# Optimization experiments

Hardware: AMD Instinct MI355X
Metric: run time of the kernel (lower is better)

## Reference

```python
import jax, jax.numpy as jnp
import numpy as np

ALPHA = 0.1        # axis_aligned_projection threshold
NEG_INF = -1e30    # large negative used for masking (softmax-equivalent to -inf)


def axis_aligned_projection(x, alpha=ALPHA):
    x_abs = jnp.abs(x)
    max_vals = jnp.max(x_abs, axis=-1, keepdims=True)
    axis_weights = jnp.where(x_abs >= alpha * max_vals, x_abs, 0.0)
    return axis_weights * jnp.sign(x)


def setup_inputs() -> dict:
    key = jax.random.key(0)
    kq, kk, kv = jax.random.split(key, 3)
    B, L, H, E = 4, 2048, 8, 64
    S, D = L, E
    queries = jax.random.normal(kq, (B, L, H, E), dtype=jnp.float32)
    keys = jax.random.normal(kk, (B, S, H, E), dtype=jnp.float32)
    values = jax.random.normal(kv, (B, S, H, D), dtype=jnp.float32)
    # TriangularCausalMask: True strictly above the diagonal -> masked out
    causal = jnp.triu(jnp.ones((L, S), dtype=jnp.bool_), k=1)
    attn_mask = jnp.broadcast_to(causal[None, None], (B, 1, L, S))
    return {"queries": queries, "keys": keys, "values": values, "attn_mask": attn_mask}


def reference(queries, keys, values, attn_mask):
    B, L, H, E = queries.shape
    scale = 1.0 / jnp.sqrt(jnp.float32(E))
    q = axis_aligned_projection(queries)
    k = axis_aligned_projection(keys)
    # [B,H,L,S] dense scores (the module materializes the full matrix)
    scores = jnp.einsum('blhe,bshe->bhls', q, k)
    scores = jnp.where(attn_mask, NEG_INF, scores)
    A = jax.nn.softmax(scale * scores, axis=-1)  # dropout is identity in eval mode
    V = jnp.einsum('bhls,bshd->blhd', A, values)
    return V
```

## Files before the change

### kernel.cpp

```cpp
#include <hip/hip_runtime.h>
#include <hip/hip_bf16.h>
#include <stdint.h>

#define B_ 4
#define L_ 2048
#define H_ 8
#define E_ 64
#define ALPHA 0.1f
#define LOG2E 1.44269504088896f
#define QSCALE (0.125f * LOG2E)
#define KSTR 72

typedef float f32x4 __attribute__((ext_vector_type(4)));
typedef short bf16x8 __attribute__((ext_vector_type(8)));
typedef short bf16x4 __attribute__((ext_vector_type(4)));
typedef uint32_t u32;
typedef unsigned short u16;
typedef u32 u32x2 __attribute__((ext_vector_type(2)));

__device__ __forceinline__ u16 f2bf(float f) {
    u32 x = __builtin_bit_cast(u32, f);
    u32 r = x + 0x7fffu + ((x >> 16) & 1u);
    return (u16)(r >> 16);
}

__device__ __forceinline__ u32 pk2bf(float a, float b) {
    u32 ua = __builtin_bit_cast(u32, a) + 0x8000u;
    u32 ub = __builtin_bit_cast(u32, b) + 0x8000u;
    return (ua >> 16) | (ub & 0xffff0000u);
}

__device__ __forceinline__ f32x4 mfma16x16x16bf16(bf16x4 a, bf16x4 b, f32x4 c) {
#if __has_builtin(__builtin_amdgcn_mfma_f32_16x16x16bf16_1k)
    return __builtin_amdgcn_mfma_f32_16x16x16bf16_1k(a, b, c, 0, 0, 0);
#elif __has_builtin(__builtin_amdgcn_mfma_f32_16x16x16_bf16)
    return __builtin_amdgcn_mfma_f32_16x16x16_bf16(a, b, c, 0, 0, 0);
#else
    f32x4 d;
    asm volatile("v_mfma_f32_16x16x16_bf16 %0, %1, %2, %3"
                 : "=v"(d) : "v"(a), "v"(b), "v"(c));
    return d;
#endif
}

__device__ __forceinline__ void dma16(const u16* g, u16* l) {
    __builtin_amdgcn_global_load_lds(
        (const __attribute__((address_space(1))) void*)g,
        (__attribute__((address_space(3))) void*)l, 16, 0, 0);
}

__global__ __launch_bounds__(256) void prep_kernel(const float* __restrict__ qin,
                                                   const float* __restrict__ kin,
                                                   const float* __restrict__ vin,
                                                   u16* __restrict__ qp,
                                                   u16* __restrict__ kp,
                                                   u16* __restrict__ vt) {
    __shared__ u16 tile[64][66];
    if (blockIdx.x < 4096) {
        const int RG = (B_ * L_ * H_) / 8;
        int wave = threadIdx.x >> 6, lane = threadIdx.x & 63;
        int g = blockIdx.x * 4 + wave;
        const float* src;
        u16* dst;
        int gr, ostr;
        float sc;
        if (g < RG) { src = qin; dst = qp; gr = g; sc = QSCALE; ostr = 64; }
        else        { src = kin; dst = kp; gr = g - RG; sc = 1.0f; ostr = KSTR; }

        int rig = lane >> 3;
        int c = (lane & 7) * 4;
        int row = gr * 8 + rig;

        const float* rp = src + (size_t)row * 64;
        float4 v0 = *(const float4*)(rp + c);
        float4 v1 = *(const float4*)(rp + c + 32);
        float f[8] = {v0.x, v0.y, v0.z, v0.w, v1.x, v1.y, v1.z, v1.w};

        float mx = 0.f;
#pragma unroll
        for (int i = 0; i < 8; ++i) mx = fmaxf(mx, fabsf(f[i]));
#pragma unroll
        for (int m = 1; m < 8; m <<= 1) mx = fmaxf(mx, __shfl_xor(mx, m));
        float thr = ALPHA * mx;

        u16 o[8];
#pragma unroll
        for (int i = 0; i < 8; ++i)
            o[i] = (fabsf(f[i]) >= thr) ? f2bf(f[i] * sc) : (u16)0;

        int b = row >> 14;
        int l = (row >> 3) & (L_ - 1);
        int h = row & 7;
        u16* orow = dst + ((size_t)(b * H_ + h) * L_ + l) * ostr;
        uint2 p0 = {(u32)o[0] | ((u32)o[1] << 16), (u32)o[2] | ((u32)o[3] << 16)};
        uint2 p1 = {(u32)o[4] | ((u32)o[5] << 16), (u32)o[6] | ((u32)o[7] << 16)};
        *(uint2*)(orow + c) = p0;
        *(uint2*)(orow + c + 32) = p1;
    } else {
        int bx = blockIdx.x - 4096;
        int bh = bx >> 5, sblk = bx & 31;
        int b = bh >> 3, h = bh & 7;
        int t = threadIdx.x;
        int s0 = sblk * 64;

#pragma unroll
        for (int p = 0; p < 2; ++p) {
            int sl = p * 32 + (t >> 3);
            int c = (t & 7) * 4;
            const float* rp = vin + (((size_t)(b * L_ + s0 + sl)) * H_ + h) * 64;
            float4 a = *(const float4*)(rp + c);
            float4 bb = *(const float4*)(rp + c + 32);
            u32* d0 = (u32*)&tile[sl][c];
            d0[0] = (u32)f2bf(a.x) | ((u32)f2bf(a.y) << 16);
            d0[1] = (u32)f2bf(a.z) | ((u32)f2bf(a.w) << 16);
            u32* d1 = (u32*)&tile[sl][c + 32];
            d1[0] = (u32)f2bf(bb.x) | ((u32)f2bf(bb.y) << 16);
            d1[1] = (u32)f2bf(bb.z) | ((u32)f2bf(bb.w) << 16);
        }
        __syncthreads();
#pragma unroll
        for (int p = 0; p < 2; ++p) {
            int d = p * 32 + (t >> 3);
            int sc2 = (t & 7) * 8;
            u16 o[8];
#pragma unroll
            for (int i = 0; i < 8; ++i) o[i] = tile[sc2 + i][d];
            uint4 val;
            val.x = (u32)o[0] | ((u32)o[1] << 16);
            val.y = (u32)o[2] | ((u32)o[3] << 16);
            val.z = (u32)o[4] | ((u32)o[5] << 16);
            val.w = (u32)o[6] | ((u32)o[7] << 16);
            *(uint4*)(vt + ((size_t)(bh * 32 + sblk) * 64 + d) * KSTR + sc2) = val;
        }
    }
}

__global__ __launch_bounds__(512, 4) void flash_kernel(const u16* __restrict__ Qp,
                                                       const u16* __restrict__ Kp,
                                                       const u16* __restrict__ Vt,
                                                       float* __restrict__ out,
                                                       float* __restrict__ pO,
                                                       float* __restrict__ pL) {
    __shared__ u16 kbuf[2][64 * KSTR];
    __shared__ u16 vbuf[2][64 * KSTR];
    int t = threadIdx.x;
    int wave = t >> 6, lane = t & 63;
    int bh = blockIdx.x & 31;
    int o5 = blockIdx.x >> 5;
    int lo = lane & 15, quad = lane >> 4;
    int b = bh >> 3, h = bh & 7;

    int group, t0, t1, slot;
    if (o5 < 8) { group = 8 + o5; t0 = 0; t1 = 15; slot = 0; }
    else {
        int p = o5 - 8;
        if ((p & 1) == 0) { group = 7 - (p >> 1);  t0 = 0;  t1 = 15 - p; slot = -1; }
        else              { group = 15 - (p >> 1); t0 = 16; t1 = 32 - p; slot = 1; }
    }
    int q0 = group * 128 + wave * 16;
    int dt = 2 * group + (wave >> 2);
    int subd = wave & 3;

    const u16* kTiles = Kp + (size_t)bh * L_ * KSTR;
    const u16* vTiles = Vt + (size_t)bh * 32 * 64 * KSTR;

    auto stage = [&](int tile, int buf) {
        const u16* kg = kTiles + (size_t)tile * 64 * KSTR;
        const u16* vg = vTiles + (size_t)tile * 64 * KSTR;
        u16* kl = kbuf[buf];
        u16* vl = vbuf[buf];
        for (int i = wave; i < 18; i += 8) {
            if (i < 9) dma16(kg + i * 512 + lane * 8, kl + i * 512);
            else       dma16(vg + (i - 9) * 512 + lane * 8, vl + (i - 9) * 512);
        }
    };

    const u16* qbase = Qp + ((size_t)bh * L_ + q0 + lo) * 64 + quad * 8;
    bf16x8 aQ0 = *(const bf16x8*)(qbase);
    bf16x8 aQ1 = *(const bf16x8*)(qbase + 32);

    f32x4 o[4];
#pragma unroll
    for (int ni = 0; ni < 4; ++ni) o[ni] = (f32x4){0.f, 0.f, 0.f, 0.f};
    float ls = 0.f;

    auto frag_proc = [&](const u16* ks, const u16* vs, int sub, bool dg) {
        bf16x8 k0 = *(const bf16x8*)(ks + (sub * 16 + lo) * KSTR + quad * 8);
        bf16x8 k1 = *(const bf16x8*)(ks + (sub * 16 + lo) * KSTR + 32 + quad * 8);
        f32x4 S = {0.f, 0.f, 0.f, 0.f};
        S = __builtin_amdgcn_mfma_f32_16x16x32_bf16(k0, aQ0, S, 0, 0, 0);
        S = __builtin_amdgcn_mfma_f32_16x16x32_bf16(k1, aQ1, S, 0, 0, 0);

        bf16x4 vf[4];
#pragma unroll
        for (int ni = 0; ni < 4; ++ni)
            vf[ni] = *(const bf16x4*)(vs + (ni * 16 + lo) * KSTR + sub * 16 + quad * 4);

        float P[4];
#pragma unroll
        for (int r = 0; r < 4; ++r) {
            float e = __builtin_amdgcn_exp2f(S[r]);
            P[r] = (dg && (quad * 4 + r > lo)) ? 0.f : e;
        }
        ls += (P[0] + P[1]) + (P[2] + P[3]);
        u32x2 pk = {pk2bf(P[0], P[1]), pk2bf(P[2], P[3])};
        bf16x4 aP = __builtin_bit_cast(bf16x4, pk);
#pragma unroll
        for (int ni = 0; ni < 4; ++ni)
            o[ni] = mfma16x16x16bf16(aP, vf[ni], o[ni]);
    };

    stage(t0, 0);
    __syncthreads();

    for (int kt = t0; kt <= t1; ++kt) {
        int cur = (kt - t0) & 1;
        if (kt < t1) stage(kt + 1, cur ^ 1);
        const u16* ks = kbuf[cur];
        const u16* vs = vbuf[cur];
        if (kt < dt) {
#pragma unroll
            for (int sub = 0; sub < 4; ++sub) frag_proc(ks, vs, sub, false);
        } else if (kt == dt) {
            for (int sub = 0; sub < subd; ++sub) frag_proc(ks, vs, sub, false);
            frag_proc(ks, vs, subd, true);
        }
        if (kt < t1) __syncthreads();
    }

    ls += __shfl_xor(ls, 16);
    ls += __shfl_xor(ls, 32);
    if (slot < 0) {
#pragma unroll
        for (int r = 0; r < 4; ++r) {
            float lr = __shfl(ls, quad * 4 + r);
            float inv = 1.0f / lr;
            int q = q0 + quad * 4 + r;
            float* ob = out + (((size_t)(b * L_ + q)) * H_ + h) * 64 + lo;
            ob[0]  = o[0][r] * inv;
            ob[16] = o[1][r] * inv;
            ob[32] = o[2][r] * inv;
            ob[48] = o[3][r] * inv;
        }
    } else {
        int gi = group - 8;
        size_t s = ((size_t)(bh * 8 + gi) * 2 + slot);
        float* po = pO + s * 8192 + (wave * 16 + quad * 4) * 64 + lo;
#pragma unroll
        for (int r = 0; r < 4; ++r) {
            po[r * 64 + 0]  = o[0][r];
            po[r * 64 + 16] = o[1][r];
            po[r * 64 + 32] = o[2][r];
            po[r * 64 + 48] = o[3][r];
        }
        if (quad == 0) pL[s * 128 + wave * 16 + lo] = ls;
    }
}

__global__ __launch_bounds__(256) void combine_kernel(const float* __restrict__ pO,
                                                      const float* __restrict__ pL,
                                                      float* __restrict__ out) {
    __shared__ float linv[128];
    int bh = blockIdx.x & 31, gi = blockIdx.x >> 5;
    int b = bh >> 3, h = bh & 7;
    int group = 8 + gi;
    int t = threadIdx.x;
    size_t sb = (size_t)(bh * 8 + gi) * 2;
    if (t < 128) linv[t] = 1.0f / (pL[sb * 128 + t] + pL[(sb + 1) * 128 + t]);
    __syncthreads();
    const float4* O1 = (const float4*)(pO + sb * 8192);
    const float4* O2 = (const float4*)(pO + (sb + 1) * 8192);
#pragma unroll
    for (int k = 0; k < 8; ++k) {
        int f4 = k * 256 + t;
        int f = f4 * 4;
        int ql = f >> 6, d = f & 63;
        float4 a = O1[f4], c = O2[f4];
        float s = linv[ql];
        float4 r = {(a.x + c.x) * s, (a.y + c.y) * s, (a.z + c.z) * s, (a.w + c.w) * s};
        int q = group * 128 + ql;
        *(float4*)(out + (((size_t)(b * L_ + q)) * H_ + h) * 64 + d) = r;
    }
}

extern "C" void kernel_launch(void* const* d_in, const int* in_sizes, int n_in,
                              void* d_out, int out_size, void* d_ws, size_t ws_size,
                              hipStream_t stream) {
    const float* q = (const float*)d_in[0];
    const float* k = (const float*)d_in[1];
    const float* v = (const float*)d_in[2];
    float* out = (float*)d_out;

    const size_t QSZ = (size_t)B_ * H_ * L_ * 64;
    const size_t KSZ = (size_t)B_ * H_ * L_ * KSTR;
    u16* qp = (u16*)d_ws;
    u16* kp = qp + QSZ;
    u16* vt = kp + KSZ;
    float* pO = (float*)(vt + KSZ);
    float* pL = pO + (size_t)32 * 8 * 2 * 8192;

    prep_kernel<<<5120, 256, 0, stream>>>(q, k, v, qp, kp, vt);
    flash_kernel<<<768, 512, 0, stream>>>(qp, kp, vt, out, pO, pL);
    combine_kernel<<<256, 256, 0, stream>>>(pO, pL, out);
}
```

Baseline: 171.2 us.

## Split causal KV range into 8-tile chunks and store partials in bf16

Replaces the two-way split-K scheme with a table-driven schedule where each block handles at most 8 KV tiles (up to 4 chunks per query group), raising the grid from 768 to 1280 blocks. This balances work more finely across CUs, so long query groups no longer set the critical path. Partial outputs are now written as bf16 rather than fp32 to cut workspace traffic, and the combine kernel sums a variable number of chunks. This adds more partial-result traffic and some precision loss in the partial accumulators.

```diff
diff --git a/kernel.cpp b/kernel.cpp
--- a/kernel.cpp
+++ b/kernel.cpp
@@ -22,6 +22,11 @@
     u32 x = __builtin_bit_cast(u32, f);
     u32 r = x + 0x7fffu + ((x >> 16) & 1u);
     return (u16)(r >> 16);
+}
+
+__device__ __forceinline__ float bf2f(u16 v) {
+    u32 x = ((u32)v) << 16;
+    return __builtin_bit_cast(float, x);
 }
 
 __device__ __forceinline__ u32 pk2bf(float a, float b) {
@@ -139,8 +144,30 @@
                                                        const u16* __restrict__ Kp,
                                                        const u16* __restrict__ Vt,
                                                        float* __restrict__ out,
-                                                       float* __restrict__ pO,
+                                                       u16* __restrict__ pO,
                                                        float* __restrict__ pL) {
+    static const unsigned char SGt[40] = {
+        3, 7, 7, 11, 11, 11, 15, 15, 15, 15,
+        4, 5, 6, 8, 8, 9, 9, 10, 10,
+        12, 12, 12, 13, 13, 13, 14, 14, 14,
+        2, 6, 10, 14,
+        1, 5, 9, 13,
+        0, 4, 8, 12};
+    static const unsigned char STt[40] = {
+        0, 0, 8, 0, 8, 16, 0, 8, 16, 24,
+        0, 0, 0, 0, 8, 0, 8, 0, 8,
+        0, 8, 16, 0, 8, 16, 0, 8, 16,
+        0, 8, 16, 24,
+        0, 8, 16, 24,
+        0, 8, 16, 24};
+    static const unsigned char SLt[40] = {
+        8, 8, 8, 8, 8, 8, 8, 8, 8, 8,
+        8, 8, 8, 8, 8, 8, 8, 8, 8,
+        8, 8, 8, 8, 8, 8, 8, 8, 8,
+        6, 6, 6, 6,
+        4, 4, 4, 4,
+        2, 2, 2, 2};
+
     __shared__ u16 kbuf[2][64 * KSTR];
     __shared__ u16 vbuf[2][64 * KSTR];
     int t = threadIdx.x;
@@ -150,13 +177,9 @@
     int lo = lane & 15, quad = lane >> 4;
     int b = bh >> 3, h = bh & 7;
 
-    int group, t0, t1, slot;
-    if (o5 < 8) { group = 8 + o5; t0 = 0; t1 = 15; slot = 0; }
-    else {
-        int p = o5 - 8;
-        if ((p & 1) == 0) { group = 7 - (p >> 1);  t0 = 0;  t1 = 15 - p; slot = -1; }
-        else              { group = 15 - (p >> 1); t0 = 16; t1 = 32 - p; slot = 1; }
-    }
+    int group = SGt[o5];
+    int t0 = STt[o5];
+    int t1 = t0 + SLt[o5] - 1;
     int q0 = group * 128 + wave * 16;
     int dt = 2 * group + (wave >> 2);
     int subd = wave & 3;
@@ -230,7 +253,7 @@
 
     ls += __shfl_xor(ls, 16);
     ls += __shfl_xor(ls, 32);
-    if (slot < 0) {
+    if (group < 4) {
 #pragma unroll
         for (int r = 0; r < 4; ++r) {
             float lr = __shfl(ls, quad * 4 + r);
@@ -243,43 +266,49 @@
             ob[48] = o[3][r] * inv;
         }
     } else {
-        int gi = group - 8;
-        size_t s = ((size_t)(bh * 8 + gi) * 2 + slot);
-        float* po = pO + s * 8192 + (wave * 16 + quad * 4) * 64 + lo;
+        int j = t0 >> 3;
+        size_t s = ((size_t)(bh * 16 + group) * 4 + j);
+        u16* po = pO + s * 8192 + (wave * 16 + quad * 4) * 64 + lo;
 #pragma unroll
         for (int r = 0; r < 4; ++r) {
-            po[r * 64 + 0]  = o[0][r];
-            po[r * 64 + 16] = o[1][r];
-            po[r * 64 + 32] = o[2][r];
-            po[r * 64 + 48] = o[3][r];
-        }
-        if (quad == 0) pL[s * 128 + wave * 16 + lo] = ls;
-    }
-}
-
-__global__ __launch_bounds__(256) void combine_kernel(const float* __restrict__ pO,
+            po[r * 64 + 0]  = f2bf(o[0][r]);
+            po[r * 64 + 16] = f2bf(o[1][r]);
+            po[r * 64 + 32] = f2bf(o[2][r]);
+            po[r * 64 + 48] = f2bf(o[3][r]);
+        }
+        if (lane < 16) pL[s * 128 + wave * 16 + lo] = ls;
+    }
+}
+
+__global__ __launch_bounds__(256) void combine_kernel(const u16* __restrict__ pO,
                                                       const float* __restrict__ pL,
                                                       float* __restrict__ out) {
     __shared__ float linv[128];
     int bh = blockIdx.x & 31, gi = blockIdx.x >> 5;
     int b = bh >> 3, h = bh & 7;
-    int group = 8 + gi;
+    int group = 4 + gi;
+    int ncg = (2 * group + 9) >> 3;
     int t = threadIdx.x;
-    size_t sb = (size_t)(bh * 8 + gi) * 2;
-    if (t < 128) linv[t] = 1.0f / (pL[sb * 128 + t] + pL[(sb + 1) * 128 + t]);
+    size_t s0 = (size_t)(bh * 16 + group) * 4;
+    if (t < 128) {
+        float l = 0.f;
+        for (int j = 0; j < ncg; ++j) l += pL[(s0 + j) * 128 + t];
+        linv[t] = 1.0f / l;
+    }
     __syncthreads();
-    const float4* O1 = (const float4*)(pO + sb * 8192);
-    const float4* O2 = (const float4*)(pO + (sb + 1) * 8192);
-#pragma unroll
-    for (int k = 0; k < 8; ++k) {
-        int f4 = k * 256 + t;
-        int f = f4 * 4;
-        int ql = f >> 6, d = f & 63;
-        float4 a = O1[f4], c = O2[f4];
-        float s = linv[ql];
-        float4 r = {(a.x + c.x) * s, (a.y + c.y) * s, (a.z + c.z) * s, (a.w + c.w) * s};
-        int q = group * 128 + ql;
-        *(float4*)(out + (((size_t)(b * L_ + q)) * H_ + h) * 64 + d) = r;
+#pragma unroll
+    for (int i = 0; i < 8; ++i) {
+        int f = (i * 256 + t) * 4;
+        int row = f >> 6, col = f & 63;
+        float a0 = 0.f, a1 = 0.f, a2 = 0.f, a3 = 0.f;
+        for (int j = 0; j < ncg; ++j) {
+            const u16* p = pO + (s0 + j) * 8192 + f;
+            a0 += bf2f(p[0]); a1 += bf2f(p[1]); a2 += bf2f(p[2]); a3 += bf2f(p[3]);
+        }
+        float s = linv[row];
+        float4 r = {a0 * s, a1 * s, a2 * s, a3 * s};
+        int q = group * 128 + row;
+        *(float4*)(out + (((size_t)(b * L_ + q)) * H_ + h) * 64 + col) = r;
     }
 }
 
@@ -296,10 +325,10 @@
     u16* qp = (u16*)d_ws;
     u16* kp = qp + QSZ;
     u16* vt = kp + KSZ;
-    float* pO = (float*)(vt + KSZ);
-    float* pL = pO + (size_t)32 * 8 * 2 * 8192;
+    u16* pO = vt + KSZ;
+    float* pL = (float*)(pO + (size_t)32 * 16 * 4 * 8192);
 
     prep_kernel<<<5120, 256, 0, stream>>>(q, k, v, qp, kp, vt);
-    flash_kernel<<<768, 512, 0, stream>>>(qp, kp, vt, out, pO, pL);
-    combine_kernel<<<256, 256, 0, stream>>>(pO, pL, out);
-}
+    flash_kernel<<<1280, 512, 0, stream>>>(qp, kp, vt, out, pO, pL);
+    combine_kernel<<<384, 256, 0, stream>>>(pO, pL, out);
+}
```

Measured after the change: 181.9 us. +6.2%, slower.
